# Kernel optimization log

Measured on AMD Instinct MI355X. Metric: run time of the kernel, lower is better.

## Reference

```python
import jax, jax.numpy as jnp
import numpy as np

N = 100000      # nodes
E = 1600000     # edges (avg degree 16)
F_IN = 512      # nfeat
C = 64          # nclass


def setup_inputs() -> dict:
    key = jax.random.key(0)
    k1, k2, k3 = jax.random.split(key, 3)
    x = jax.random.normal(k1, (N, F_IN), dtype=jnp.float32)
    edge_index = jax.random.randint(k2, (2, E), 0, N, dtype=jnp.int32)
    # GCNConv weight (glorot-ish) and bias
    W = jax.random.normal(k3, (F_IN, C), dtype=jnp.float32) * (1.0 / np.sqrt(F_IN))
    b = jnp.zeros((C,), dtype=jnp.float32)
    return {"x": x, "W": W, "b": b, "edge_index": edge_index}


def reference(x, W, b, edge_index):
    # Standard GCNConv (sheaf_laplacian=None): project, add self-loops,
    # symmetric normalization D^{-1/2}(A+I)D^{-1/2}, aggregate, bias.
    h = x @ W  # [N, C] project first (C < F_IN), as torch_geometric does
    self_loops = jnp.arange(N, dtype=edge_index.dtype)
    src = jnp.concatenate([edge_index[0], self_loops])
    dst = jnp.concatenate([edge_index[1], self_loops])
    deg = jax.ops.segment_sum(jnp.ones_like(dst, dtype=h.dtype), dst, num_segments=N)
    dinv = jnp.where(deg > 0, jax.lax.rsqrt(deg), 0.0)  # deg^{-1/2}
    norm = dinv[src] * dinv[dst]  # [E+N]
    msgs = h[src] * norm[:, None]  # gather + scale, [E+N, C]
    out = jax.ops.segment_sum(msgs, dst, num_segments=N) + b  # [N, C]
    return jax.nn.log_softmax(out, axis=1)
```

## Files before the change

### kernel.cpp

```cpp
#include <hip/hip_runtime.h>
#include <hip/hip_bf16.h>

#define F_IN 512
#define NCLS 64
#define SCAN_BLK 512
#define CNT_STRIDE 16

typedef __attribute__((ext_vector_type(8))) short short8;
typedef __attribute__((ext_vector_type(4))) float f32x4;

static __device__ __forceinline__ short bf16_of(float f) {
    __hip_bfloat16 h = __float2bfloat16(f);
    short s;
    __builtin_memcpy(&s, &h, 2);
    return s;
}
static __device__ __forceinline__ float b2f(short s) {
    unsigned u = ((unsigned)(unsigned short)s) << 16;
    float f;
    __builtin_memcpy(&f, &u, 4);
    return f;
}

__global__ __launch_bounds__(256) void k_prelude(const float* __restrict__ W,
                                                 short* __restrict__ Wb,
                                                 int* __restrict__ cnt, int nWords) {
    const int bid = blockIdx.x;
    if (bid < 16) {
        int t = bid * 256 + threadIdx.x;
        int c = t >> 10;
        int kk = (t >> 6) & 15;
        int l = t & 63;
        short8 v;
#pragma unroll
        for (int j = 0; j < 8; ++j) {
            v[j] = bf16_of(W[(size_t)(kk * 32 + (l >> 4) * 8 + j) * NCLS + c * 16 + (l & 15)]);
        }
        reinterpret_cast<short8*>(Wb)[t] = v;
    } else {
        int i = ((bid - 16) * 256 + threadIdx.x) * 4;
        if (i + 4 <= nWords) {
            *reinterpret_cast<int4*>(cnt + i) = make_int4(0, 0, 0, 0);
        } else {
            for (int k2 = i; k2 < nWords; ++k2) cnt[k2] = 0;
        }
    }
}

__global__ __launch_bounds__(256) void k_deg(const int* __restrict__ dst,
                                             int* __restrict__ cnt,
                                             unsigned short* __restrict__ rank, int e) {
    int base = (blockIdx.x * 256 + threadIdx.x) * 8;
    if (base + 8 <= e) {
        int4 dA = *reinterpret_cast<const int4*>(dst + base);
        int4 dB = *reinterpret_cast<const int4*>(dst + base + 4);
        ushort4 rA, rB;
        rA.x = (unsigned short)atomicAdd(&cnt[dA.x * CNT_STRIDE], 1);
        rA.y = (unsigned short)atomicAdd(&cnt[dA.y * CNT_STRIDE], 1);
        rA.z = (unsigned short)atomicAdd(&cnt[dA.z * CNT_STRIDE], 1);
        rA.w = (unsigned short)atomicAdd(&cnt[dA.w * CNT_STRIDE], 1);
        rB.x = (unsigned short)atomicAdd(&cnt[dB.x * CNT_STRIDE], 1);
        rB.y = (unsigned short)atomicAdd(&cnt[dB.y * CNT_STRIDE], 1);
        rB.z = (unsigned short)atomicAdd(&cnt[dB.z * CNT_STRIDE], 1);
        rB.w = (unsigned short)atomicAdd(&cnt[dB.w * CNT_STRIDE], 1);
        *reinterpret_cast<ushort4*>(rank + base) = rA;
        *reinterpret_cast<ushort4*>(rank + base + 4) = rB;
    } else {
        for (int i = base; i < e; ++i)
            rank[i] = (unsigned short)atomicAdd(&cnt[dst[i] * CNT_STRIDE], 1);
    }
}

__global__ __launch_bounds__(SCAN_BLK) void k_scan1(const int* __restrict__ cnt,
                                                    int* __restrict__ off,
                                                    int* __restrict__ partials,
                                                    float* __restrict__ dinv, int n) {
    __shared__ int s[SCAN_BLK];
    int tid = threadIdx.x;
    int i = blockIdx.x * SCAN_BLK + tid;
    int v = (i < n) ? cnt[i * CNT_STRIDE] : 0;
    if (i < n) dinv[i] = rsqrtf(1.0f + (float)v);
    s[tid] = v;
    __syncthreads();
#pragma unroll
    for (int d = 1; d < SCAN_BLK; d <<= 1) {
        int t = (tid >= d) ? s[tid - d] : 0;
        __syncthreads();
        s[tid] += t;
        __syncthreads();
    }
    if (i < n) off[i] = s[tid] - v;
    if (i == n - 1) off[n] = s[tid];
    if (tid == SCAN_BLK - 1) partials[blockIdx.x] = s[tid];
}

__global__ __launch_bounds__(256) void k_scan2(int* __restrict__ partials, int p) {
    __shared__ int s[256];
    int tid = threadIdx.x;
    int v = (tid < p) ? partials[tid] : 0;
    s[tid] = v;
    __syncthreads();
#pragma unroll
    for (int d = 1; d < 256; d <<= 1) {
        int t = (tid >= d) ? s[tid - d] : 0;
        __syncthreads();
        s[tid] += t;
        __syncthreads();
    }
    if (tid < p) partials[tid] = s[tid] - v;
}

__global__ __launch_bounds__(256) void k_fill(const int* __restrict__ src,
                                              const int* __restrict__ dst,
                                              const int* __restrict__ off,
                                              const int* __restrict__ parts,
                                              const unsigned short* __restrict__ rank,
                                              int* __restrict__ eidx, int e) {
    int base = (blockIdx.x * 256 + threadIdx.x) * 4;
    if (base + 4 <= e) {
        int4 s4 = *reinterpret_cast<const int4*>(src + base);
        int4 d4 = *reinterpret_cast<const int4*>(dst + base);
        ushort4 r4 = *reinterpret_cast<const ushort4*>(rank + base);
        eidx[off[d4.x] + parts[d4.x >> 9] + r4.x] = s4.x;
        eidx[off[d4.y] + parts[d4.y >> 9] + r4.y] = s4.y;
        eidx[off[d4.z] + parts[d4.z >> 9] + r4.z] = s4.z;
        eidx[off[d4.w] + parts[d4.w >> 9] + r4.w] = s4.w;
    } else {
        for (int i = base; i < e; ++i)
            eidx[off[dst[i]] + parts[dst[i] >> 9] + rank[i]] = src[i];
    }
}

__global__ __launch_bounds__(256) void k_gemm(const float* __restrict__ x,
                                              const short* __restrict__ Wb,
                                              const float* __restrict__ dinv,
                                              short* __restrict__ g, int n) {
    const int wave = threadIdx.x >> 6;
    const int lane = threadIdx.x & 63;
    const int rowTile = blockIdx.x * 128 + wave * 32;

    int r0 = rowTile + (lane & 15);
    int r1 = r0 + 16;
    if (r0 > n - 1) r0 = n - 1;
    if (r1 > n - 1) r1 = n - 1;
    const float* xr0 = x + (size_t)r0 * F_IN + ((lane >> 4) * 8);
    const float* xr1 = x + (size_t)r1 * F_IN + ((lane >> 4) * 8);

    const short8* wb8 = reinterpret_cast<const short8*>(Wb);

    f32x4 acc[2][4];
#pragma unroll
    for (int h = 0; h < 2; ++h)
#pragma unroll
        for (int c = 0; c < 4; ++c) acc[h][c] = {0.f, 0.f, 0.f, 0.f};

#pragma unroll 4
    for (int kk = 0; kk < 16; ++kk) {
        float4 p0 = *reinterpret_cast<const float4*>(xr0 + kk * 32);
        float4 p1 = *reinterpret_cast<const float4*>(xr0 + kk * 32 + 4);
        float4 q0 = *reinterpret_cast<const float4*>(xr1 + kk * 32);
        float4 q1 = *reinterpret_cast<const float4*>(xr1 + kk * 32 + 4);
        short8 a0, a1;
        a0[0] = bf16_of(p0.x); a0[1] = bf16_of(p0.y);
        a0[2] = bf16_of(p0.z); a0[3] = bf16_of(p0.w);
        a0[4] = bf16_of(p1.x); a0[5] = bf16_of(p1.y);
        a0[6] = bf16_of(p1.z); a0[7] = bf16_of(p1.w);
        a1[0] = bf16_of(q0.x); a1[1] = bf16_of(q0.y);
        a1[2] = bf16_of(q0.z); a1[3] = bf16_of(q0.w);
        a1[4] = bf16_of(q1.x); a1[5] = bf16_of(q1.y);
        a1[6] = bf16_of(q1.z); a1[7] = bf16_of(q1.w);
        short8 b0 = wb8[(0 * 16 + kk) * 64 + lane];
        short8 b1 = wb8[(1 * 16 + kk) * 64 + lane];
        short8 b2 = wb8[(2 * 16 + kk) * 64 + lane];
        short8 b3 = wb8[(3 * 16 + kk) * 64 + lane];
        acc[0][0] = __builtin_amdgcn_mfma_f32_16x16x32_bf16(a0, b0, acc[0][0], 0, 0, 0);
        acc[0][1] = __builtin_amdgcn_mfma_f32_16x16x32_bf16(a0, b1, acc[0][1], 0, 0, 0);
        acc[0][2] = __builtin_amdgcn_mfma_f32_16x16x32_bf16(a0, b2, acc[0][2], 0, 0, 0);
        acc[0][3] = __builtin_amdgcn_mfma_f32_16x16x32_bf16(a0, b3, acc[0][3], 0, 0, 0);
        acc[1][0] = __builtin_amdgcn_mfma_f32_16x16x32_bf16(a1, b0, acc[1][0], 0, 0, 0);
        acc[1][1] = __builtin_amdgcn_mfma_f32_16x16x32_bf16(a1, b1, acc[1][1], 0, 0, 0);
        acc[1][2] = __builtin_amdgcn_mfma_f32_16x16x32_bf16(a1, b2, acc[1][2], 0, 0, 0);
        acc[1][3] = __builtin_amdgcn_mfma_f32_16x16x32_bf16(a1, b3, acc[1][3], 0, 0, 0);
    }

    const int col = lane & 15;
#pragma unroll
    for (int h = 0; h < 2; ++h) {
        const int rbase = rowTile + h * 16 + (lane >> 4) * 4;
#pragma unroll
        for (int j = 0; j < 4; ++j) {
            int r = rbase + j;
            if (r < n) {
                float dv = dinv[r];
                short* go = g + (size_t)r * NCLS + col;
                go[0]  = bf16_of(acc[h][0][j] * dv);
                go[16] = bf16_of(acc[h][1][j] * dv);
                go[32] = bf16_of(acc[h][2][j] * dv);
                go[48] = bf16_of(acc[h][3][j] * dv);
            }
        }
    }
}

__global__ __launch_bounds__(256) void k_agg(const short* __restrict__ g,
                                             const float* __restrict__ dinv,
                                             const float* __restrict__ bvec,
                                             const int* __restrict__ off,
                                             const int* __restrict__ parts,
                                             const int* __restrict__ eidx,
                                             float* __restrict__ out, int n) {
    const int wave = threadIdx.x >> 6;
    const int lane = threadIdx.x & 63;
    const int grp = lane >> 3;
    const int li = lane & 7;
    const int node = (blockIdx.x * 4 + wave) * 8 + grp;
    if (node >= n) return;

    const int s0 = off[node] + parts[node >> 9];
    const int np1 = node + 1;
    const int s1 = off[np1] + parts[(np1 == n ? n - 1 : np1) >> 9];

    const short8* g8 = reinterpret_cast<const short8*>(g);

    float acc[8];
    {
        short8 v = g8[(size_t)node * 8 + li];
#pragma unroll
        for (int c = 0; c < 8; ++c) acc[c] = b2f(v[c]);
    }

    int t = s0;
    for (; t + 8 <= s1; t += 8) {
        int sidx[8];
#pragma unroll
        for (int u = 0; u < 8; ++u) sidx[u] = eidx[t + u];
        short8 vv[8];
#pragma unroll
        for (int u = 0; u < 8; ++u) vv[u] = g8[(size_t)sidx[u] * 8 + li];
#pragma unroll
        for (int c = 0; c < 8; ++c)
            acc[c] += ((b2f(vv[0][c]) + b2f(vv[1][c])) + (b2f(vv[2][c]) + b2f(vv[3][c]))) +
                      ((b2f(vv[4][c]) + b2f(vv[5][c])) + (b2f(vv[6][c]) + b2f(vv[7][c])));
    }
    for (; t + 4 <= s1; t += 4) {
        int sa = eidx[t], sb = eidx[t + 1], sc = eidx[t + 2], sd = eidx[t + 3];
        short8 va = g8[(size_t)sa * 8 + li];
        short8 vb = g8[(size_t)sb * 8 + li];
        short8 vc = g8[(size_t)sc * 8 + li];
        short8 vd = g8[(size_t)sd * 8 + li];
#pragma unroll
        for (int c = 0; c < 8; ++c)
            acc[c] += (b2f(va[c]) + b2f(vb[c])) + (b2f(vc[c]) + b2f(vd[c]));
    }
    for (; t < s1; ++t) {
        int sa = eidx[t];
        short8 va = g8[(size_t)sa * 8 + li];
#pragma unroll
        for (int c = 0; c < 8; ++c) acc[c] += b2f(va[c]);
    }

    const float dn = dinv[node];
    const float4 b0 = reinterpret_cast<const float4*>(bvec)[li * 2];
    const float4 b1 = reinterpret_cast<const float4*>(bvec)[li * 2 + 1];
    float v[8];
    v[0] = acc[0] * dn + b0.x; v[1] = acc[1] * dn + b0.y;
    v[2] = acc[2] * dn + b0.z; v[3] = acc[3] * dn + b0.w;
    v[4] = acc[4] * dn + b1.x; v[5] = acc[5] * dn + b1.y;
    v[6] = acc[6] * dn + b1.z; v[7] = acc[7] * dn + b1.w;

    float m = v[0];
#pragma unroll
    for (int c = 1; c < 8; ++c) m = fmaxf(m, v[c]);
#pragma unroll
    for (int o = 1; o < 8; o <<= 1) m = fmaxf(m, __shfl_xor(m, o));

    float ex = 0.f;
#pragma unroll
    for (int c = 0; c < 8; ++c) ex += __expf(v[c] - m);
#pragma unroll
    for (int o = 1; o < 8; o <<= 1) ex += __shfl_xor(ex, o);
    const float lg = m + __logf(ex);

    float4 r0, r1;
    r0.x = v[0] - lg; r0.y = v[1] - lg; r0.z = v[2] - lg; r0.w = v[3] - lg;
    r1.x = v[4] - lg; r1.y = v[5] - lg; r1.z = v[6] - lg; r1.w = v[7] - lg;
    float4* o4 = reinterpret_cast<float4*>(out + (size_t)node * NCLS);
    o4[li * 2] = r0;
    o4[li * 2 + 1] = r1;
}

extern "C" void kernel_launch(void* const* d_in, const int* in_sizes, int n_in,
                              void* d_out, int out_size, void* d_ws, size_t ws_size,
                              hipStream_t stream) {
    const float* x = (const float*)d_in[0];
    const float* W = (const float*)d_in[1];
    const float* b = (const float*)d_in[2];
    const int* edge_index = (const int*)d_in[3];

    const int N = in_sizes[0] / F_IN;
    const int E = in_sizes[3] / 2;
    const int* src = edge_index;
    const int* dst = edge_index + E;

    float* out = (float*)d_out;

    char* ws = (char*)d_ws;
    short* g     = (short*)ws;  ws += (size_t)N * NCLS * 2;
    short* Wb    = (short*)ws;  ws += 4096 * 16;
    float* dinv  = (float*)ws;  ws += (size_t)N * 4;
    int*   cnt   = (int*)ws;    ws += (size_t)N * CNT_STRIDE * 4;
    int*   off   = (int*)ws;    ws += (size_t)(N + 4) * 4;
    int*   parts = (int*)ws;    ws += 1024 * 4;
    unsigned short* rank = (unsigned short*)ws;  ws += (size_t)((E + 7) & ~7) * 2;
    int*   eidx  = (int*)ws;

    const int nWords = N * CNT_STRIDE;
    const int nScanBlocks = (N + SCAN_BLK - 1) / SCAN_BLK;
    const int fillBlocks = (E + 1023) / 1024;
    const int degBlocks = (E + 2047) / 2048;

    k_prelude<<<16 + (nWords / 4 + 255) / 256, 256, 0, stream>>>(W, Wb, cnt, nWords);

    k_deg<<<degBlocks, 256, 0, stream>>>(dst, cnt, rank, E);

    k_scan1<<<nScanBlocks, SCAN_BLK, 0, stream>>>(cnt, off, parts, dinv, N);
    k_scan2<<<1, 256, 0, stream>>>(parts, nScanBlocks);

    k_gemm<<<(N + 127) / 128, 256, 0, stream>>>(x, Wb, dinv, g, N);

    k_fill<<<fillBlocks, 256, 0, stream>>>(src, dst, off, parts, rank, eidx, E);

    k_agg<<<(N + 31) / 32, 256, 0, stream>>>(g, dinv, b, off, parts, eidx, out, N);
}
```

Measured before the change: 186.9 us.

## Aggregate one node per wave with edge-split lanes; shrink rank to bytes

k_agg now assigns a whole wave to one node, with eight lane groups striding over its edges and combining partial sums by cross-lane shuffles, to cut per-node serial gather latency and degree imbalance. The rank array is narrowed to 8-bit to reduce traffic in the degree and fill kernels, and fill uses non-temporal stores for the scattered CSR writes. The byte rank assumes in-degree below 256, and the grid for aggregation grows eightfold with most lanes idle at the epilogue.

```diff
diff --git a/kernel.cpp b/kernel.cpp
--- a/kernel.cpp
+++ b/kernel.cpp
@@ -49,25 +49,25 @@
 
 __global__ __launch_bounds__(256) void k_deg(const int* __restrict__ dst,
                                              int* __restrict__ cnt,
-                                             unsigned short* __restrict__ rank, int e) {
+                                             unsigned char* __restrict__ rank, int e) {
     int base = (blockIdx.x * 256 + threadIdx.x) * 8;
     if (base + 8 <= e) {
         int4 dA = *reinterpret_cast<const int4*>(dst + base);
         int4 dB = *reinterpret_cast<const int4*>(dst + base + 4);
-        ushort4 rA, rB;
-        rA.x = (unsigned short)atomicAdd(&cnt[dA.x * CNT_STRIDE], 1);
-        rA.y = (unsigned short)atomicAdd(&cnt[dA.y * CNT_STRIDE], 1);
-        rA.z = (unsigned short)atomicAdd(&cnt[dA.z * CNT_STRIDE], 1);
-        rA.w = (unsigned short)atomicAdd(&cnt[dA.w * CNT_STRIDE], 1);
-        rB.x = (unsigned short)atomicAdd(&cnt[dB.x * CNT_STRIDE], 1);
-        rB.y = (unsigned short)atomicAdd(&cnt[dB.y * CNT_STRIDE], 1);
-        rB.z = (unsigned short)atomicAdd(&cnt[dB.z * CNT_STRIDE], 1);
-        rB.w = (unsigned short)atomicAdd(&cnt[dB.w * CNT_STRIDE], 1);
-        *reinterpret_cast<ushort4*>(rank + base) = rA;
-        *reinterpret_cast<ushort4*>(rank + base + 4) = rB;
+        uchar4 rA, rB;
+        rA.x = (unsigned char)atomicAdd(&cnt[dA.x * CNT_STRIDE], 1);
+        rA.y = (unsigned char)atomicAdd(&cnt[dA.y * CNT_STRIDE], 1);
+        rA.z = (unsigned char)atomicAdd(&cnt[dA.z * CNT_STRIDE], 1);
+        rA.w = (unsigned char)atomicAdd(&cnt[dA.w * CNT_STRIDE], 1);
+        rB.x = (unsigned char)atomicAdd(&cnt[dB.x * CNT_STRIDE], 1);
+        rB.y = (unsigned char)atomicAdd(&cnt[dB.y * CNT_STRIDE], 1);
+        rB.z = (unsigned char)atomicAdd(&cnt[dB.z * CNT_STRIDE], 1);
+        rB.w = (unsigned char)atomicAdd(&cnt[dB.w * CNT_STRIDE], 1);
+        *reinterpret_cast<uchar4*>(rank + base) = rA;
+        *reinterpret_cast<uchar4*>(rank + base + 4) = rB;
     } else {
         for (int i = base; i < e; ++i)
-            rank[i] = (unsigned short)atomicAdd(&cnt[dst[i] * CNT_STRIDE], 1);
+            rank[i] = (unsigned char)atomicAdd(&cnt[dst[i] * CNT_STRIDE], 1);
     }
 }
 
@@ -114,20 +114,21 @@
                                               const int* __restrict__ dst,
                                               const int* __restrict__ off,
                                               const int* __restrict__ parts,
-                                              const unsigned short* __restrict__ rank,
+                                              const unsigned char* __restrict__ rank,
                                               int* __restrict__ eidx, int e) {
     int base = (blockIdx.x * 256 + threadIdx.x) * 4;
     if (base + 4 <= e) {
         int4 s4 = *reinterpret_cast<const int4*>(src + base);
         int4 d4 = *reinterpret_cast<const int4*>(dst + base);
-        ushort4 r4 = *reinterpret_cast<const ushort4*>(rank + base);
-        eidx[off[d4.x] + parts[d4.x >> 9] + r4.x] = s4.x;
-        eidx[off[d4.y] + parts[d4.y >> 9] + r4.y] = s4.y;
-        eidx[off[d4.z] + parts[d4.z >> 9] + r4.z] = s4.z;
-        eidx[off[d4.w] + parts[d4.w >> 9] + r4.w] = s4.w;
+        uchar4 r4 = *reinterpret_cast<const uchar4*>(rank + base);
+        __builtin_nontemporal_store(s4.x, &eidx[off[d4.x] + parts[d4.x >> 9] + r4.x]);
+        __builtin_nontemporal_store(s4.y, &eidx[off[d4.y] + parts[d4.y >> 9] + r4.y]);
+        __builtin_nontemporal_store(s4.z, &eidx[off[d4.z] + parts[d4.z >> 9] + r4.z]);
+        __builtin_nontemporal_store(s4.w, &eidx[off[d4.w] + parts[d4.w >> 9] + r4.w]);
     } else {
         for (int i = base; i < e; ++i)
-            eidx[off[dst[i]] + parts[dst[i] >> 9] + rank[i]] = src[i];
+            __builtin_nontemporal_store(src[i],
+                &eidx[off[dst[i]] + parts[dst[i] >> 9] + rank[i]]);
     }
 }
 
@@ -211,9 +212,9 @@
                                              float* __restrict__ out, int n) {
     const int wave = threadIdx.x >> 6;
     const int lane = threadIdx.x & 63;
-    const int grp = lane >> 3;
+    const int u = lane >> 3;
     const int li = lane & 7;
-    const int node = (blockIdx.x * 4 + wave) * 8 + grp;
+    const int node = blockIdx.x * 4 + wave;
     if (node >= n) return;
 
     const int s0 = off[node] + parts[node >> 9];
@@ -223,40 +224,36 @@
     const short8* g8 = reinterpret_cast<const short8*>(g);
 
     float acc[8];
-    {
+    if (u == 0) {
         short8 v = g8[(size_t)node * 8 + li];
 #pragma unroll
         for (int c = 0; c < 8; ++c) acc[c] = b2f(v[c]);
-    }
-
-    int t = s0;
-    for (; t + 8 <= s1; t += 8) {
-        int sidx[8];
-#pragma unroll
-        for (int u = 0; u < 8; ++u) sidx[u] = eidx[t + u];
-        short8 vv[8];
-#pragma unroll
-        for (int u = 0; u < 8; ++u) vv[u] = g8[(size_t)sidx[u] * 8 + li];
-#pragma unroll
-        for (int c = 0; c < 8; ++c)
-            acc[c] += ((b2f(vv[0][c]) + b2f(vv[1][c])) + (b2f(vv[2][c]) + b2f(vv[3][c]))) +
-                      ((b2f(vv[4][c]) + b2f(vv[5][c])) + (b2f(vv[6][c]) + b2f(vv[7][c])));
-    }
-    for (; t + 4 <= s1; t += 4) {
-        int sa = eidx[t], sb = eidx[t + 1], sc = eidx[t + 2], sd = eidx[t + 3];
+    } else {
+#pragma unroll
+        for (int c = 0; c < 8; ++c) acc[c] = 0.f;
+    }
+
+    int t = s0 + u;
+    for (; t + 8 < s1; t += 16) {
+        int sa = eidx[t];
+        int sb = eidx[t + 8];
         short8 va = g8[(size_t)sa * 8 + li];
         short8 vb = g8[(size_t)sb * 8 + li];
-        short8 vc = g8[(size_t)sc * 8 + li];
-        short8 vd = g8[(size_t)sd * 8 + li];
-#pragma unroll
-        for (int c = 0; c < 8; ++c)
-            acc[c] += (b2f(va[c]) + b2f(vb[c])) + (b2f(vc[c]) + b2f(vd[c]));
-    }
-    for (; t < s1; ++t) {
+#pragma unroll
+        for (int c = 0; c < 8; ++c) acc[c] += b2f(va[c]) + b2f(vb[c]);
+    }
+    if (t < s1) {
         int sa = eidx[t];
         short8 va = g8[(size_t)sa * 8 + li];
 #pragma unroll
         for (int c = 0; c < 8; ++c) acc[c] += b2f(va[c]);
+    }
+
+#pragma unroll
+    for (int c = 0; c < 8; ++c) {
+        acc[c] += __shfl_xor(acc[c], 8);
+        acc[c] += __shfl_xor(acc[c], 16);
+        acc[c] += __shfl_xor(acc[c], 32);
     }
 
     const float dn = dinv[node];
@@ -281,12 +278,14 @@
     for (int o = 1; o < 8; o <<= 1) ex += __shfl_xor(ex, o);
     const float lg = m + __logf(ex);
 
-    float4 r0, r1;
-    r0.x = v[0] - lg; r0.y = v[1] - lg; r0.z = v[2] - lg; r0.w = v[3] - lg;
-    r1.x = v[4] - lg; r1.y = v[5] - lg; r1.z = v[6] - lg; r1.w = v[7] - lg;
-    float4* o4 = reinterpret_cast<float4*>(out + (size_t)node * NCLS);
-    o4[li * 2] = r0;
-    o4[li * 2 + 1] = r1;
+    if (u == 0) {
+        float4 r0, r1;
+        r0.x = v[0] - lg; r0.y = v[1] - lg; r0.z = v[2] - lg; r0.w = v[3] - lg;
+        r1.x = v[4] - lg; r1.y = v[5] - lg; r1.z = v[6] - lg; r1.w = v[7] - lg;
+        float4* o4 = reinterpret_cast<float4*>(out + (size_t)node * NCLS);
+        o4[li * 2] = r0;
+        o4[li * 2 + 1] = r1;
+    }
 }
 
 extern "C" void kernel_launch(void* const* d_in, const int* in_sizes, int n_in,
@@ -311,7 +310,7 @@
     int*   cnt   = (int*)ws;    ws += (size_t)N * CNT_STRIDE * 4;
     int*   off   = (int*)ws;    ws += (size_t)(N + 4) * 4;
     int*   parts = (int*)ws;    ws += 1024 * 4;
-    unsigned short* rank = (unsigned short*)ws;  ws += (size_t)((E + 7) & ~7) * 2;
+    unsigned char* rank = (unsigned char*)ws;  ws += (size_t)((E + 15) & ~15);
     int*   eidx  = (int*)ws;
 
     const int nWords = N * CNT_STRIDE;
@@ -330,5 +329,5 @@
 
     k_fill<<<fillBlocks, 256, 0, stream>>>(src, dst, off, parts, rank, eidx, E);
 
-    k_agg<<<(N + 31) / 32, 256, 0, stream>>>(g, dinv, b, off, parts, eidx, out, N);
-}
+    k_agg<<<(N + 3) / 4, 256, 0, stream>>>(g, dinv, b, off, parts, eidx, out, N);
+}
```

Result: slower. 220.3 us (+17.9%).
